# Kernel tuning notes

Hardware: AMD Instinct MI355X
Metric: run time of the kernel (lower is better)

## Reference

```python
import jax, jax.numpy as jnp
import numpy as np

NUM_CONN = 8

def _ein_reduce(f):
    # Einstein t-norm fold over last axis: T(a,b) = ab / (2 - (a+b-ab))
    acc = f[..., 0]
    for i in range(1, f.shape[-1]):
        b = f[..., i]
        ab = acc * b
        acc = ab / (2.0 - (acc + b - ab))
    return acc

def _coein_reduce(f):
    # Einstein t-conorm fold over last axis: S(a,b) = (a+b) / (1 + ab)
    acc = f[..., 0]
    for i in range(1, f.shape[-1]):
        b = f[..., i]
        acc = (acc + b) / (1.0 + acc * b)
    return acc

def _ddlg_layer(x, w, idx, is_train):
    # x: [B, in], idx: [out, C] int, w: [out, 4]
    feats = x[:, idx]                      # [B, out, C] gather
    ops = jnp.stack([
        jnp.min(feats, axis=-1),
        jnp.max(feats, axis=-1),
        _ein_reduce(feats),
        _coein_reduce(feats),
    ], axis=-1)                            # [B, out, 4]
    if is_train:
        prob = jax.nn.softmax(w, axis=-1)  # [out, 4]
    else:
        prob = jax.nn.one_hot(jnp.argmax(w, axis=-1), 4, dtype=x.dtype)
    return jnp.einsum('bof,of->bo', ops, prob)

def setup_inputs() -> dict:
    key = jax.random.key(0)
    ks = jax.random.split(key, 6)
    sizes = [4096, 2048, 1024, 2048, 4096]
    x = jax.random.uniform(ks[0], (4096, sizes[0]), dtype=jnp.float32)
    ws = [jax.random.normal(ks[1 + i], (sizes[i + 1], 4), dtype=jnp.float32) for i in range(4)]
    rng = np.random.default_rng(0)
    idxs = []
    for i in range(4):
        # randperm-without-replacement per output neuron
        perm = np.argsort(rng.random((sizes[i + 1], sizes[i])), axis=-1)[:, :NUM_CONN]
        idxs.append(jnp.asarray(perm, dtype=jnp.int32))
    return {
        'x': x,
        'w0': ws[0], 'w1': ws[1], 'w2': ws[2], 'w3': ws[3],
        'idx0': idxs[0], 'idx1': idxs[1], 'idx2': idxs[2], 'idx3': idxs[3],
        'is_train': 1,
    }

def reference(x, w0, w1, w2, w3, idx0, idx1, idx2, idx3, is_train):
    h = _ddlg_layer(x, w0, idx0, is_train)
    h = _ddlg_layer(h, w1, idx1, is_train)
    h = _ddlg_layer(h, w2, idx2, is_train)
    h = _ddlg_layer(h, w3, idx3, is_train)
    return h
```

## Files before the change

kernel.cpp:

```cpp
#include <hip/hip_runtime.h>


#define BATCH 4096

typedef _Float16 h2 __attribute__((ext_vector_type(2)));
typedef _Float16 h4 __attribute__((ext_vector_type(4)));

__device__ __forceinline__ float fastrcp(float x) { return __builtin_amdgcn_rcpf(x); }
__device__ __forceinline__ _Float16 hrcp(_Float16 x) {
#if __has_builtin(__builtin_amdgcn_rcph)
    return __builtin_amdgcn_rcph(x);
#else
    return (_Float16)__builtin_amdgcn_rcpf((float)x);
#endif
}

__global__ __launch_bounds__(256) void prep_k(const float* __restrict__ w0,
                                              const float* __restrict__ w1,
                                              const float* __restrict__ w2,
                                              const float* __restrict__ w3,
                                              const int* __restrict__ is_train,
                                              h4* __restrict__ probsH) {
    const int g = blockIdx.x * 256 + threadIdx.x;
    const float* w; int o;
    if (g < 2048)      { w = w0; o = g; }
    else if (g < 3072) { w = w1; o = g - 2048; }
    else if (g < 5120) { w = w2; o = g - 3072; }
    else               { w = w3; o = g - 5120; }
    float wv[4];
#pragma unroll
    for (int c = 0; c < 4; ++c) wv[c] = w[(o << 2) + c];
    float p[4];
    if (*is_train) {
        float m = fmaxf(fmaxf(wv[0], wv[1]), fmaxf(wv[2], wv[3]));
        float s = 0.0f;
#pragma unroll
        for (int c = 0; c < 4; ++c) { p[c] = __expf(wv[c] - m); s += p[c]; }
        float inv = fastrcp(s);
#pragma unroll
        for (int c = 0; c < 4; ++c) p[c] *= inv;
    } else {
        int a = 0; float best = wv[0];
#pragma unroll
        for (int c = 1; c < 4; ++c) if (wv[c] > best) { best = wv[c]; a = c; }
#pragma unroll
        for (int c = 0; c < 4; ++c) p[c] = (c == a) ? 1.0f : 0.0f;
    }
    probsH[g] = h4{(_Float16)p[0], (_Float16)p[1], (_Float16)p[2], (_Float16)p[3]};
}

struct Raw { h2 lo, hi; };

__device__ __forceinline__ Raw row_at(const uint2* __restrict__ rows, int i) {
    const uint2 v = rows[i];
    Raw r;
    r.lo = __builtin_bit_cast(h2, v.x);
    r.hi = __builtin_bit_cast(h2, v.y);
    return r;
}
__device__ __forceinline__ h2 splat2(_Float16 s) { h2 v = {s, s}; return v; }

struct Chain { h2 mn0, mn1, mx0, mx1, De0, De1, Ne0, Ne1, Nc0, Nc1, Dc0, Dc1; };

__device__ __forceinline__ void cinit(Chain& C, Raw v) {
    const h2 one = splat2((_Float16)1.0f), two = splat2((_Float16)2.0f);
    C.mn0 = v.lo; C.mx0 = v.lo; C.De0 = v.lo;
    C.Ne0 = two - v.lo; C.Nc0 = one + v.lo; C.Dc0 = one - v.lo;
    C.mn1 = v.hi; C.mx1 = v.hi; C.De1 = v.hi;
    C.Ne1 = two - v.hi; C.Nc1 = one + v.hi; C.Dc1 = one - v.hi;
}
__device__ __forceinline__ void cstep(Chain& C, Raw v) {
    const h2 two = splat2((_Float16)2.0f);
    C.mn0 = __builtin_elementwise_min(C.mn0, v.lo);
    C.mn1 = __builtin_elementwise_min(C.mn1, v.hi);
    C.mx0 = __builtin_elementwise_max(C.mx0, v.lo);
    C.mx1 = __builtin_elementwise_max(C.mx1, v.hi);
    C.De0 *= v.lo;            C.De1 *= v.hi;
    C.Ne0 *= (two - v.lo);    C.Ne1 *= (two - v.hi);
    C.Nc0 += C.Nc0 * v.lo;    C.Nc1 += C.Nc1 * v.hi;
    C.Dc0 -= C.Dc0 * v.lo;    C.Dc1 -= C.Dc1 * v.hi;
}
__device__ __forceinline__ Raw finale(const Chain& C, h4 P) {
    h2 s10 = C.Ne0 + C.De0, s11 = C.Ne1 + C.De1;
    h2 s20 = C.Nc0 + C.Dc0, s21 = C.Nc1 + C.Dc1;
    h2 d10 = C.Nc0 - C.Dc0, d11 = C.Nc1 - C.Dc1;
    h2 ss0 = s10 * s20,     ss1 = s11 * s21;
    h2 r0 = {hrcp(ss0[0]), hrcp(ss0[1])};
    h2 r1 = {hrcp(ss1[0]), hrcp(ss1[1])};
    h2 t10 = (C.De0 + C.De0) * s20, t11 = (C.De1 + C.De1) * s21;
    h2 t20 = d10 * s10,             t21 = d11 * s11;
    const h2 P0 = splat2(P[0]), P1 = splat2(P[1]);
    const h2 P2 = splat2(P[2]), P3 = splat2(P[3]);
    h2 num0 = P2 * t10 + P3 * t20;
    h2 num1 = P2 * t11 + P3 * t21;
    Raw res;
    res.lo = P0 * C.mn0 + P1 * C.mx0 + num0 * r0;
    res.hi = P0 * C.mn1 + P1 * C.mx1 + num1 * r1;
    return res;
}

__device__ __forceinline__ Raw gate1(const uint2* __restrict__ rows,
                                     const int4* __restrict__ idx,
                                     const h4* __restrict__ probs, int o) {
    const int4 i0 = idx[o * 2], i1 = idx[o * 2 + 1];
    const h4 P = probs[o];
    Raw A[8];
    A[0] = row_at(rows, i0.x); A[1] = row_at(rows, i0.y);
    A[2] = row_at(rows, i0.z); A[3] = row_at(rows, i0.w);
    A[4] = row_at(rows, i1.x); A[5] = row_at(rows, i1.y);
    A[6] = row_at(rows, i1.z); A[7] = row_at(rows, i1.w);
    Chain C; cinit(C, A[0]);
#pragma unroll
    for (int c = 1; c < 8; ++c) cstep(C, A[c]);
    return finale(C, P);
}

__device__ __forceinline__ void gate2(const uint2* __restrict__ rows,
                                      const int4* __restrict__ idx,
                                      const h4* __restrict__ probs,
                                      int o0, Raw& ra, Raw& rb) {
    const int4 a0 = idx[o0 * 2],     a1 = idx[o0 * 2 + 1];
    const int4 b0 = idx[o0 * 2 + 2], b1 = idx[o0 * 2 + 3];
    const h4 PA = probs[o0], PB = probs[o0 + 1];
    Raw A[8], B[8];
    A[0] = row_at(rows, a0.x); A[1] = row_at(rows, a0.y);
    A[2] = row_at(rows, a0.z); A[3] = row_at(rows, a0.w);
    A[4] = row_at(rows, a1.x); A[5] = row_at(rows, a1.y);
    A[6] = row_at(rows, a1.z); A[7] = row_at(rows, a1.w);
    B[0] = row_at(rows, b0.x); B[1] = row_at(rows, b0.y);
    B[2] = row_at(rows, b0.z); B[3] = row_at(rows, b0.w);
    B[4] = row_at(rows, b1.x); B[5] = row_at(rows, b1.y);
    B[6] = row_at(rows, b1.z); B[7] = row_at(rows, b1.w);
    Chain CA, CB;
    cinit(CA, A[0]);
    cinit(CB, B[0]);
#pragma unroll
    for (int c = 1; c < 8; ++c) {
        cstep(CA, A[c]);
        cstep(CB, B[c]);
    }
    ra = finale(CA, PA);
    rb = finale(CB, PB);
}

__device__ __forceinline__ uint2 raw_bits(Raw r) {
    return uint2{__builtin_bit_cast(unsigned, r.lo), __builtin_bit_cast(unsigned, r.hi)};
}

__global__ __launch_bounds__(1024, 8) void ddlg_fused(const float* __restrict__ x,
                                                      const h4* __restrict__ probsH,
                                                      const int4* __restrict__ idx0,
                                                      const int4* __restrict__ idx1,
                                                      const int4* __restrict__ idx2,
                                                      const int4* __restrict__ idx3,
                                                      float* __restrict__ out) {
    __shared__ __align__(16) _Float16 lds[24576];
    const int t  = threadIdx.x;
    const int b0 = blockIdx.x << 2;

    const uint2* xl  = (const uint2*)lds;
    const uint2* h0v = (const uint2*)(lds + 16384);
    const uint2* h1v = (const uint2*)lds;
    const uint2* h2v = (const uint2*)(lds + 16384);

#pragma unroll
    for (int c = 0; c < 4; ++c) {
        const int j = (c << 10) + t;
        const float v0 = x[(size_t)(b0 + 0) * 4096 + j];
        const float v1 = x[(size_t)(b0 + 1) * 4096 + j];
        const float v2 = x[(size_t)(b0 + 2) * 4096 + j];
        const float v3 = x[(size_t)(b0 + 3) * 4096 + j];
        h2 a = {(_Float16)v0, (_Float16)v1};
        h2 b = {(_Float16)v2, (_Float16)v3};
        uint2 hv = {__builtin_bit_cast(unsigned, a), __builtin_bit_cast(unsigned, b)};
        *(uint2*)(lds + (j << 2)) = hv;
    }
    __syncthreads();

    {
        Raw ra, rb;
        gate2(xl, idx0, probsH, 2 * t, ra, rb);
        uint2 ua = raw_bits(ra), ub = raw_bits(rb);
        *(uint4*)(lds + 16384 + (t << 3)) = uint4{ua.x, ua.y, ub.x, ub.y};
    }
    __syncthreads();

    {
        Raw r = gate1(h0v, idx1, probsH + 2048, t);
        *(uint2*)(lds + (t << 2)) = raw_bits(r);
    }
    __syncthreads();

    {
        Raw ra, rb;
        gate2(h1v, idx2, probsH + 3072, 2 * t, ra, rb);
        uint2 ua = raw_bits(ra), ub = raw_bits(rb);
        *(uint4*)(lds + 16384 + (t << 3)) = uint4{ua.x, ua.y, ub.x, ub.y};
    }
    __syncthreads();

    {
        Raw r0, r1, r2, r3;
        gate2(h2v, idx3, probsH + 5120, 4 * t,     r0, r1);
        gate2(h2v, idx3, probsH + 5120, 4 * t + 2, r2, r3);
        float4 o4;
        o4 = make_float4((float)r0.lo[0], (float)r1.lo[0], (float)r2.lo[0], (float)r3.lo[0]);
        *(float4*)(out + (size_t)(b0 + 0) * 4096 + (t << 2)) = o4;
        o4 = make_float4((float)r0.lo[1], (float)r1.lo[1], (float)r2.lo[1], (float)r3.lo[1]);
        *(float4*)(out + (size_t)(b0 + 1) * 4096 + (t << 2)) = o4;
        o4 = make_float4((float)r0.hi[0], (float)r1.hi[0], (float)r2.hi[0], (float)r3.hi[0]);
        *(float4*)(out + (size_t)(b0 + 2) * 4096 + (t << 2)) = o4;
        o4 = make_float4((float)r0.hi[1], (float)r1.hi[1], (float)r2.hi[1], (float)r3.hi[1]);
        *(float4*)(out + (size_t)(b0 + 3) * 4096 + (t << 2)) = o4;
    }
}

extern "C" void kernel_launch(void* const* d_in, const int* in_sizes, int n_in,
                              void* d_out, int out_size, void* d_ws, size_t ws_size,
                              hipStream_t stream) {
    const float* x        = (const float*)d_in[0];
    const float* w0       = (const float*)d_in[1];
    const float* w1       = (const float*)d_in[2];
    const float* w2       = (const float*)d_in[3];
    const float* w3       = (const float*)d_in[4];
    const int4*  idx0     = (const int4*)d_in[5];
    const int4*  idx1     = (const int4*)d_in[6];
    const int4*  idx2     = (const int4*)d_in[7];
    const int4*  idx3     = (const int4*)d_in[8];
    const int*   is_train = (const int*)d_in[9];
    float*       out      = (float*)d_out;

    h4* probsH = (h4*)d_ws;

    prep_k<<<36, 256, 0, stream>>>(w0, w1, w2, w3, is_train, probsH);
    ddlg_fused<<<1024, 1024, 0, stream>>>(x, probsH, idx0, idx1, idx2, idx3, out);
}
```

Before: 165.5 us.

## Fuse softmax prep into main kernel and shrink blocks to 512 threads

```diff
diff --git a/kernel.cpp b/kernel.cpp
--- a/kernel.cpp
+++ b/kernel.cpp
@@ -4,7 +4,6 @@
 #define BATCH 4096
 
 typedef _Float16 h2 __attribute__((ext_vector_type(2)));
-typedef _Float16 h4 __attribute__((ext_vector_type(4)));
 
 __device__ __forceinline__ float fastrcp(float x) { return __builtin_amdgcn_rcpf(x); }
 __device__ __forceinline__ _Float16 hrcp(_Float16 x) {
@@ -14,39 +13,29 @@
     return (_Float16)__builtin_amdgcn_rcpf((float)x);
 #endif
 }
-
-__global__ __launch_bounds__(256) void prep_k(const float* __restrict__ w0,
-                                              const float* __restrict__ w1,
-                                              const float* __restrict__ w2,
-                                              const float* __restrict__ w3,
-                                              const int* __restrict__ is_train,
-                                              h4* __restrict__ probsH) {
-    const int g = blockIdx.x * 256 + threadIdx.x;
-    const float* w; int o;
-    if (g < 2048)      { w = w0; o = g; }
-    else if (g < 3072) { w = w1; o = g - 2048; }
-    else if (g < 5120) { w = w2; o = g - 3072; }
-    else               { w = w3; o = g - 5120; }
-    float wv[4];
-#pragma unroll
-    for (int c = 0; c < 4; ++c) wv[c] = w[(o << 2) + c];
-    float p[4];
-    if (*is_train) {
-        float m = fmaxf(fmaxf(wv[0], wv[1]), fmaxf(wv[2], wv[3]));
-        float s = 0.0f;
-#pragma unroll
-        for (int c = 0; c < 4; ++c) { p[c] = __expf(wv[c] - m); s += p[c]; }
-        float inv = fastrcp(s);
-#pragma unroll
-        for (int c = 0; c < 4; ++c) p[c] *= inv;
+__device__ __forceinline__ h2 splat2(_Float16 s) { h2 v = {s, s}; return v; }
+
+__device__ __forceinline__ void probs_of(const float* __restrict__ w, int o,
+                                         bool train, _Float16 P[4]) {
+    const float4 wv = ((const float4*)w)[o];
+    float v0 = wv.x, v1 = wv.y, v2 = wv.z, v3 = wv.w;
+    if (train) {
+        float m = fmaxf(fmaxf(v0, v1), fmaxf(v2, v3));
+        float e0 = __expf(v0 - m), e1 = __expf(v1 - m);
+        float e2 = __expf(v2 - m), e3 = __expf(v3 - m);
+        float inv = fastrcp(e0 + e1 + e2 + e3);
+        P[0] = (_Float16)(e0 * inv); P[1] = (_Float16)(e1 * inv);
+        P[2] = (_Float16)(e2 * inv); P[3] = (_Float16)(e3 * inv);
     } else {
-        int a = 0; float best = wv[0];
-#pragma unroll
-        for (int c = 1; c < 4; ++c) if (wv[c] > best) { best = wv[c]; a = c; }
-#pragma unroll
-        for (int c = 0; c < 4; ++c) p[c] = (c == a) ? 1.0f : 0.0f;
-    }
-    probsH[g] = h4{(_Float16)p[0], (_Float16)p[1], (_Float16)p[2], (_Float16)p[3]};
+        int a = 0; float best = v0;
+        if (v1 > best) { best = v1; a = 1; }
+        if (v2 > best) { best = v2; a = 2; }
+        if (v3 > best) { best = v3; a = 3; }
+        P[0] = (_Float16)(a == 0 ? 1.0f : 0.0f);
+        P[1] = (_Float16)(a == 1 ? 1.0f : 0.0f);
+        P[2] = (_Float16)(a == 2 ? 1.0f : 0.0f);
+        P[3] = (_Float16)(a == 3 ? 1.0f : 0.0f);
+    }
 }
 
 struct Raw { h2 lo, hi; };
@@ -58,7 +47,9 @@
     r.hi = __builtin_bit_cast(h2, v.y);
     return r;
 }
-__device__ __forceinline__ h2 splat2(_Float16 s) { h2 v = {s, s}; return v; }
+__device__ __forceinline__ uint2 raw_bits(Raw r) {
+    return uint2{__builtin_bit_cast(unsigned, r.lo), __builtin_bit_cast(unsigned, r.hi)};
+}
 
 struct Chain { h2 mn0, mn1, mx0, mx1, De0, De1, Ne0, Ne1, Nc0, Nc1, Dc0, Dc1; };
 
@@ -80,7 +71,7 @@
     C.Nc0 += C.Nc0 * v.lo;    C.Nc1 += C.Nc1 * v.hi;
     C.Dc0 -= C.Dc0 * v.lo;    C.Dc1 -= C.Dc1 * v.hi;
 }
-__device__ __forceinline__ Raw finale(const Chain& C, h4 P) {
+__device__ __forceinline__ Raw finale(const Chain& C, const _Float16 P[4]) {
     h2 s10 = C.Ne0 + C.De0, s11 = C.Ne1 + C.De1;
     h2 s20 = C.Nc0 + C.Dc0, s21 = C.Nc1 + C.Dc1;
     h2 d10 = C.Nc0 - C.Dc0, d11 = C.Nc1 - C.Dc1;
@@ -99,11 +90,13 @@
     return res;
 }
 
-__device__ __forceinline__ Raw gate1(const uint2* __restrict__ rows,
-                                     const int4* __restrict__ idx,
-                                     const h4* __restrict__ probs, int o) {
+__device__ __forceinline__ Raw gate(const uint2* __restrict__ rows,
+                                    const int4* __restrict__ idx,
+                                    const float* __restrict__ w,
+                                    bool train, int o) {
     const int4 i0 = idx[o * 2], i1 = idx[o * 2 + 1];
-    const h4 P = probs[o];
+    _Float16 P[4];
+    probs_of(w, o, train, P);
     Raw A[8];
     A[0] = row_at(rows, i0.x); A[1] = row_at(rows, i0.y);
     A[2] = row_at(rows, i0.z); A[3] = row_at(rows, i0.w);
@@ -115,48 +108,21 @@
     return finale(C, P);
 }
 
-__device__ __forceinline__ void gate2(const uint2* __restrict__ rows,
-                                      const int4* __restrict__ idx,
-                                      const h4* __restrict__ probs,
-                                      int o0, Raw& ra, Raw& rb) {
-    const int4 a0 = idx[o0 * 2],     a1 = idx[o0 * 2 + 1];
-    const int4 b0 = idx[o0 * 2 + 2], b1 = idx[o0 * 2 + 3];
-    const h4 PA = probs[o0], PB = probs[o0 + 1];
-    Raw A[8], B[8];
-    A[0] = row_at(rows, a0.x); A[1] = row_at(rows, a0.y);
-    A[2] = row_at(rows, a0.z); A[3] = row_at(rows, a0.w);
-    A[4] = row_at(rows, a1.x); A[5] = row_at(rows, a1.y);
-    A[6] = row_at(rows, a1.z); A[7] = row_at(rows, a1.w);
-    B[0] = row_at(rows, b0.x); B[1] = row_at(rows, b0.y);
-    B[2] = row_at(rows, b0.z); B[3] = row_at(rows, b0.w);
-    B[4] = row_at(rows, b1.x); B[5] = row_at(rows, b1.y);
-    B[6] = row_at(rows, b1.z); B[7] = row_at(rows, b1.w);
-    Chain CA, CB;
-    cinit(CA, A[0]);
-    cinit(CB, B[0]);
-#pragma unroll
-    for (int c = 1; c < 8; ++c) {
-        cstep(CA, A[c]);
-        cstep(CB, B[c]);
-    }
-    ra = finale(CA, PA);
-    rb = finale(CB, PB);
-}
-
-__device__ __forceinline__ uint2 raw_bits(Raw r) {
-    return uint2{__builtin_bit_cast(unsigned, r.lo), __builtin_bit_cast(unsigned, r.hi)};
-}
-
-__global__ __launch_bounds__(1024, 8) void ddlg_fused(const float* __restrict__ x,
-                                                      const h4* __restrict__ probsH,
-                                                      const int4* __restrict__ idx0,
-                                                      const int4* __restrict__ idx1,
-                                                      const int4* __restrict__ idx2,
-                                                      const int4* __restrict__ idx3,
-                                                      float* __restrict__ out) {
+__global__ __launch_bounds__(512, 6) void ddlg_fused(const float* __restrict__ x,
+                                                     const float* __restrict__ w0,
+                                                     const float* __restrict__ w1,
+                                                     const float* __restrict__ w2,
+                                                     const float* __restrict__ w3,
+                                                     const int* __restrict__ is_train,
+                                                     const int4* __restrict__ idx0,
+                                                     const int4* __restrict__ idx1,
+                                                     const int4* __restrict__ idx2,
+                                                     const int4* __restrict__ idx3,
+                                                     float* __restrict__ out) {
     __shared__ __align__(16) _Float16 lds[24576];
     const int t  = threadIdx.x;
     const int b0 = blockIdx.x << 2;
+    const bool train = (*is_train) != 0;
 
     const uint2* xl  = (const uint2*)lds;
     const uint2* h0v = (const uint2*)(lds + 16384);
@@ -164,8 +130,8 @@
     const uint2* h2v = (const uint2*)(lds + 16384);
 
 #pragma unroll
-    for (int c = 0; c < 4; ++c) {
-        const int j = (c << 10) + t;
+    for (int c = 0; c < 8; ++c) {
+        const int j = (c << 9) + t;
         const float v0 = x[(size_t)(b0 + 0) * 4096 + j];
         const float v1 = x[(size_t)(b0 + 1) * 4096 + j];
         const float v2 = x[(size_t)(b0 + 2) * 4096 + j];
@@ -177,41 +143,38 @@
     }
     __syncthreads();
 
-    {
-        Raw ra, rb;
-        gate2(xl, idx0, probsH, 2 * t, ra, rb);
-        uint2 ua = raw_bits(ra), ub = raw_bits(rb);
-        *(uint4*)(lds + 16384 + (t << 3)) = uint4{ua.x, ua.y, ub.x, ub.y};
-    }
-    __syncthreads();
-
-    {
-        Raw r = gate1(h0v, idx1, probsH + 2048, t);
-        *(uint2*)(lds + (t << 2)) = raw_bits(r);
-    }
-    __syncthreads();
-
-    {
-        Raw ra, rb;
-        gate2(h1v, idx2, probsH + 3072, 2 * t, ra, rb);
-        uint2 ua = raw_bits(ra), ub = raw_bits(rb);
-        *(uint4*)(lds + 16384 + (t << 3)) = uint4{ua.x, ua.y, ub.x, ub.y};
-    }
-    __syncthreads();
-
-    {
-        Raw r0, r1, r2, r3;
-        gate2(h2v, idx3, probsH + 5120, 4 * t,     r0, r1);
-        gate2(h2v, idx3, probsH + 5120, 4 * t + 2, r2, r3);
-        float4 o4;
-        o4 = make_float4((float)r0.lo[0], (float)r1.lo[0], (float)r2.lo[0], (float)r3.lo[0]);
-        *(float4*)(out + (size_t)(b0 + 0) * 4096 + (t << 2)) = o4;
-        o4 = make_float4((float)r0.lo[1], (float)r1.lo[1], (float)r2.lo[1], (float)r3.lo[1]);
-        *(float4*)(out + (size_t)(b0 + 1) * 4096 + (t << 2)) = o4;
-        o4 = make_float4((float)r0.hi[0], (float)r1.hi[0], (float)r2.hi[0], (float)r3.hi[0]);
-        *(float4*)(out + (size_t)(b0 + 2) * 4096 + (t << 2)) = o4;
-        o4 = make_float4((float)r0.hi[1], (float)r1.hi[1], (float)r2.hi[1], (float)r3.hi[1]);
-        *(float4*)(out + (size_t)(b0 + 3) * 4096 + (t << 2)) = o4;
+#pragma unroll
+    for (int k = 0; k < 4; ++k) {
+        const int o = (k << 9) + t;
+        Raw r = gate(xl, idx0, w0, train, o);
+        *(uint2*)(lds + 16384 + (o << 2)) = raw_bits(r);
+    }
+    __syncthreads();
+
+#pragma unroll
+    for (int k = 0; k < 2; ++k) {
+        const int o = (k << 9) + t;
+        Raw r = gate(h0v, idx1, w1, train, o);
+        *(uint2*)(lds + (o << 2)) = raw_bits(r);
+    }
+    __syncthreads();
+
+#pragma unroll
+    for (int k = 0; k < 4; ++k) {
+        const int o = (k << 9) + t;
+        Raw r = gate(h1v, idx2, w2, train, o);
+        *(uint2*)(lds + 16384 + (o << 2)) = raw_bits(r);
+    }
+    __syncthreads();
+
+#pragma unroll
+    for (int k = 0; k < 8; ++k) {
+        const int o = (k << 9) + t;
+        Raw r = gate(h2v, idx3, w3, train, o);
+        out[(size_t)(b0 + 0) * 4096 + o] = (float)r.lo[0];
+        out[(size_t)(b0 + 1) * 4096 + o] = (float)r.lo[1];
+        out[(size_t)(b0 + 2) * 4096 + o] = (float)r.hi[0];
+        out[(size_t)(b0 + 3) * 4096 + o] = (float)r.hi[1];
     }
 }
 
@@ -230,8 +193,8 @@
     const int*   is_train = (const int*)d_in[9];
     float*       out      = (float*)d_out;
 
-    h4* probsH = (h4*)d_ws;
-
-    prep_k<<<36, 256, 0, stream>>>(w0, w1, w2, w3, is_train, probsH);
-    ddlg_fused<<<1024, 1024, 0, stream>>>(x, probsH, idx0, idx1, idx2, idx3, out);
-}
+    (void)d_ws; (void)ws_size;
+
+    ddlg_fused<<<1024, 512, 0, stream>>>(x, w0, w1, w2, w3, is_train,
+                                         idx0, idx1, idx2, idx3, out);
+}
```

Result: no change. 167.5 us (+1.2%).
